# Kernel optimization log

Hardware: AMD Instinct MI355X
Metric: run time of the kernel (lower is better)

## Reference

```python
import jax, jax.numpy as jnp
import numpy as np
from jax import lax

BN_EPS = 1e-5
TINY = 1e-12


def conv2d(x, w, stride, padding):
    # NCHW x OIHW -> NCHW
    return lax.conv_general_dilated(
        x, w, (stride, stride), [(padding, padding), (padding, padding)],
        dimension_numbers=('NCHW', 'OIHW', 'NCHW'))


def pool2x2(x):
    B, C, H, W = x.shape
    return x.reshape(B, C, H // 2, 2, W // 2, 2).mean(axis=(3, 5))


def setup_inputs() -> dict:
    key = jax.random.key(0)
    k0, k1, k2, k3 = jax.random.split(key, 4)
    B, Cin, H, W = 32, 128, 56, 56
    Cout, K = 256, 3
    mean = jax.random.normal(k0, (B, Cin, H, W), jnp.float32)
    std = jax.random.uniform(k1, (B, Cin, H, W), jnp.float32)  # std must be >= 0
    fan_in = Cin * K * K
    bound = 1.0 / np.sqrt(fan_in)  # torch Conv2d default init
    conv_w = jax.random.uniform(k2, (Cout, Cin, K, K), jnp.float32, -bound, bound)
    conv_b = jax.random.uniform(k3, (Cout,), jnp.float32, -bound, bound)
    bn_gamma = jnp.full((Cout,), 2.5, jnp.float32)  # module fills weight with 2.5
    bn_beta = jnp.full((Cout,), 2.5, jnp.float32)   # module fills bias with 2.5
    return {'mean': mean, 'std': std, 'conv_w': conv_w, 'conv_b': conv_b,
            'bn_gamma': bn_gamma, 'bn_beta': bn_beta}


def reference(mean, std, conv_w, conv_b, bn_gamma, bn_beta):
    # mean branch: standard conv
    m = conv2d(mean, conv_w, 1, 1) + conv_b[None, :, None, None]
    # std branch (no rho): independent-variance propagation, var -> conv with w^2
    var = conv2d(std * std, conv_w * conv_w, 1, 1)
    s = jnp.sqrt(var + TINY)
    # BatchNorm2d in training mode: batch statistics over (N, H, W)
    mu = jnp.mean(m, axis=(0, 2, 3), keepdims=True)
    v = jnp.var(m, axis=(0, 2, 3), keepdims=True)  # biased, like torch normalization
    inv = 1.0 / jnp.sqrt(v + BN_EPS)
    g = bn_gamma[None, :, None, None]
    uhat = (m - mu) * inv * g + bn_beta[None, :, None, None]
    # std through BN: pure linear scale by |gamma| / sqrt(var + eps)
    shat = s * inv * jnp.abs(g)
    # moment activation (erf-based Gaussian->Heaviside moment mapping)
    z = uhat / (shat * np.sqrt(2.0) + TINY)
    u = 0.5 * (1.0 + lax.erf(z))               # output mean in (0, 1)
    sa = jnp.sqrt(jnp.clip(u * (1.0 - u), TINY))  # output std of Bernoulli-like moments
    # avg-pool 2x2 stride 2: mean pools linearly, independent vars: std = sqrt(avg(var))/2
    u_p = pool2x2(u)
    s_p = jnp.sqrt(pool2x2(sa * sa)) * 0.5
    return (u_p, s_p)
```

## Files before the change

### kernel.cpp

```cpp
#include <hip/hip_runtime.h>
#include <hip/hip_bf16.h>
#include <math.h>

#define BB 32
#define CIN 128
#define HH 56
#define WW 56
#define COUT 256
#define HW (HH*WW)
#define NPIX (BB*HW)
#define PH 28
#define PW 28
#define POOL_ELEMS ((long)BB*COUT*PH*PW)
#define PADH 58
#define PADW 58
#define ROW_BLOCKS (BB*HH)
#define TOPBOT_BLOCKS (BB*2)
#define WPACK_BLOCKS ((9*COUT*CIN)/256)

typedef unsigned short u16;
using s16x8 = __attribute__((ext_vector_type(8))) short;
using s16x4 = __attribute__((ext_vector_type(4))) short;
using f32x4 = __attribute__((ext_vector_type(4))) float;

__device__ __forceinline__ float b2f(u16 u){ return __uint_as_float(((unsigned)u)<<16); }
__device__ __forceinline__ u16 f2b(float x){
    unsigned u = __float_as_uint(x);
    unsigned r = (u + 0x7fffu + ((u>>16)&1u)) >> 16;
    return (u16)r;
}

__device__ __forceinline__ void gload16(const void* g, void* l){
    __builtin_amdgcn_global_load_lds(
        (const __attribute__((address_space(1))) unsigned int*)g,
        (__attribute__((address_space(3))) unsigned int*)l, 16, 0, 0);
}


__global__ __launch_bounds__(256) void prep_kernel(
    const float* __restrict__ mean, const float* __restrict__ stdv,
    const float* __restrict__ w,
    u16* __restrict__ mean_pad, u16* __restrict__ std2_pad,
    u16* __restrict__ BP, u16* __restrict__ BP2,
    float* __restrict__ sum_, float* __restrict__ sumsq_)
{
    const int bid = blockIdx.x;
    const int t   = threadIdx.x;

    if (bid < ROW_BLOCKS){
        __shared__ u16 ldsm[56*128];
        __shared__ u16 ldss[56*128];
        const int b = bid / HH;
        const int h = bid - b*HH;

        #pragma unroll
        for (int k=0; k<7; ++k){
            int idx = k*256 + t;
            int c   = idx / 14;
            int f4  = idx - c*14;
            long ga = ((long)(b*CIN + c)*HH + h)*WW + f4*4;
            const f32x4 m4 = *(const f32x4*)(mean + ga);
            const f32x4 s4 = *(const f32x4*)(stdv + ga);
            #pragma unroll
            for (int j=0; j<4; ++j){
                int px = f4*4 + j;
                int ci = px*128 + (c ^ ((px & 15) << 3));
                ldsm[ci] = f2b(m4[j]);
                ldss[ci] = f2b(s4[j] * s4[j]);
            }
        }
        __syncthreads();

        const long rowbase = ((long)(b*PADH + (h+1)))*PADW*CIN;
        #pragma unroll
        for (int k=0; k<4; ++k){
            int slot = k*256 + t;
            int px   = slot >> 4;
            int oct  = slot & 15;
            if (px < 56){
                int ci = px*128 + ((oct ^ (px & 15)) << 3);
                long o = rowbase + (long)(px+1)*CIN + oct*8;
                *(s16x8*)(mean_pad + o) = *(const s16x8*)&ldsm[ci];
                *(s16x8*)(std2_pad + o) = *(const s16x8*)&ldss[ci];
            }
        }
        if (t < 64){
            int buf = t >> 5;
            int ppx = ((t >> 4) & 1) ? 57 : 0;
            int oct = t & 15;
            long o  = rowbase + (long)ppx*CIN + oct*8;
            s16x8 z = (s16x8){0,0,0,0,0,0,0,0};
            *(s16x8*)((buf ? std2_pad : mean_pad) + o) = z;
        }
    } else if (bid < ROW_BLOCKS + TOPBOT_BLOCKS){
        int row = bid - ROW_BLOCKS;
        int b   = row >> 1;
        int ph  = (row & 1) ? (PADH-1) : 0;
        const long rowbase = ((long)(b*PADH + ph))*PADW*CIN;
        s16x8 z = (s16x8){0,0,0,0,0,0,0,0};
        #pragma unroll
        for (int k=0; k<8; ++k){
            int g = k*256 + t;
            if (g < 2*PADW*16){
                int buf = g >= PADW*16;
                int gg  = buf ? g - PADW*16 : g;
                int px  = gg >> 4;
                int oct = gg & 15;
                long o  = rowbase + (long)px*CIN + oct*8;
                *(s16x8*)((buf ? std2_pad : mean_pad) + o) = z;
            }
        }
        if (row == 0){ sum_[t] = 0.f; sumsq_[t] = 0.f; }
    } else {
        int tt = (bid - ROW_BLOCKS - TOPBOT_BLOCKS)*256 + t;
        int e    = tt & 7;
        int co   = (tt >> 3) & 255;
        int rest = tt >> 11;
        int ks   = rest >> 2;
        int sub  = rest & 3;
        int r    = ks >> 2;
        int ci   = (ks & 3)*32 + sub*8 + e;
        float v = w[((long)co*CIN + ci)*9 + r];
        BP[tt]  = f2b(v);
        BP2[tt] = f2b(v*v);
    }
}

__global__ __launch_bounds__(256,2) void convw_kernel(
    const u16* __restrict__ mean_pad, const u16* __restrict__ std2_pad,
    const u16* __restrict__ BP, const u16* __restrict__ BP2,
    const float* __restrict__ bias,
    u16* __restrict__ m_out, u16* __restrict__ v_out,
    float* __restrict__ sum_, float* __restrict__ sumsq_)
{
    __shared__ u16 lds[32768];
    const int tid  = threadIdx.x;
    const int lane = tid & 63;
    const int wv   = tid >> 6;

    int gid   = blockIdx.x;
    int local = gid >> 3;
    int p     = (gid & 7)*112 + (local >> 1);
    int path  = local & 1;
    const int b  = p / 28;
    const int h0 = (p - b*28) * 2;

    const u16* __restrict__ Ap = path ? std2_pad : mean_pad;
    const u16* __restrict__ Bp = path ? BP2      : BP;
    u16*       __restrict__ Op = path ? v_out    : m_out;

    const int slot_g = (tid & 15) ^ ((tid >> 4) & 15);
    const int wbase  = (b*PADH + h0)*PADW*CIN;
    const int athr   = (tid >> 4)*CIN + slot_g*8;
    #pragma unroll
    for (int i=0; i<16; ++i){
        const int Ci = (i>>2)*(PADW*CIN) + (i&3)*16*CIN;
        gload16(Ap + wbase + Ci + athr, &lds[i*2048 + tid*8]);
    }
    __syncthreads();

    int R0[7];
    #pragma unroll
    for (int mi=0; mi<7; ++mi){
        int px = mi*16 + (lane & 15);
        int dh = (px >= 56) ? 1 : 0;
        R0[mi] = dh*64 + (px - dh*56);
    }
    const int q = lane >> 4;

    const u16* bp = Bp + (size_t)((lane>>4)*256 + wv*64 + (lane&15))*8;

    f32x4 acc[7][4];
    #pragma unroll
    for (int i=0;i<7;i++)
      #pragma unroll
      for (int j=0;j<4;j++) acc[i][j] = (f32x4){0,0,0,0};

    #pragma unroll
    for (int r=0; r<9; ++r){
        const int kh = r/3, kw = r - (r/3)*3;

        int ab[7];
        #pragma unroll
        for (int mi=0; mi<7; ++mi){
            int R   = R0[mi] + kh*64 + kw;
            int t15 = (R0[mi] + kw) & 15;
            ab[mi] = R*128 + ((q ^ t15) << 3);
        }

        #pragma unroll
        for (int hf=0; hf<2; ++hf){
            #pragma unroll
            for (int kk=0; kk<2; ++kk){
                const size_t ksoff = (size_t)(r*4 + hf*2 + kk)*8192;
                s16x8 bf0 = *(const s16x8*)(bp + ksoff);
                s16x8 bf1 = *(const s16x8*)(bp + ksoff + 128);
                s16x8 bf2 = *(const s16x8*)(bp + ksoff + 256);
                s16x8 bf3 = *(const s16x8*)(bp + ksoff + 384);
                const int sx = hf*64 + kk*32;
                s16x8 af[7];
                #pragma unroll
                for (int mi=0; mi<7; ++mi)
                    af[mi] = *(const s16x8*)&lds[ab[mi] ^ sx];
                __builtin_amdgcn_s_setprio(1);
                #pragma unroll
                for (int mi=0; mi<7; ++mi){
                    acc[mi][0] = __builtin_amdgcn_mfma_f32_16x16x32_bf16(af[mi], bf0, acc[mi][0], 0,0,0);
                    acc[mi][1] = __builtin_amdgcn_mfma_f32_16x16x32_bf16(af[mi], bf1, acc[mi][1], 0,0,0);
                    acc[mi][2] = __builtin_amdgcn_mfma_f32_16x16x32_bf16(af[mi], bf2, acc[mi][2], 0,0,0);
                    acc[mi][3] = __builtin_amdgcn_mfma_f32_16x16x32_bf16(af[mi], bf3, acc[mi][3], 0,0,0);
                }
                __builtin_amdgcn_s_setprio(0);
            }
        }
    }

    float bv[4];
    if (path == 0){
        #pragma unroll
        for (int ni=0;ni<4;ni++) bv[ni] = bias[wv*64 + ni*16 + (lane&15)];
    } else {
        #pragma unroll
        for (int ni=0;ni<4;ni++) bv[ni] = 0.f;
    }

    float ssum[4] = {0.f,0.f,0.f,0.f}, ssq[4] = {0.f,0.f,0.f,0.f};

    #pragma unroll
    for (int mi=0; mi<7; ++mi){
        int px = mi*16 + ((lane>>4)<<2);
        int dh = (px >= 56) ? 1 : 0;
        int w  = px - dh*56;
        #pragma unroll
        for (int ni=0; ni<4; ++ni){
            int co = wv*64 + ni*16 + (lane&15);
            size_t o = (size_t)(b*COUT + co)*HW + (size_t)(h0+dh)*WW + w;
            s16x4 pk;
            #pragma unroll
            for (int rr=0; rr<4; ++rr){
                float vv = acc[mi][ni][rr] + bv[ni];
                pk[rr] = (short)f2b(vv);
                ssum[ni] += vv;
                ssq[ni]  += vv*vv;
            }
            *(s16x4*)(Op + o) = pk;
        }
    }

    if (path == 0){
        #pragma unroll
        for (int ni=0; ni<4; ++ni){
            float s = ssum[ni], s2 = ssq[ni];
            s  += __shfl_xor(s, 16, 64);  s2 += __shfl_xor(s2, 16, 64);
            s  += __shfl_xor(s, 32, 64);  s2 += __shfl_xor(s2, 32, 64);
            if (lane < 16){
                int co = wv*64 + ni*16 + lane;
                atomicAdd(&sum_[co],   s);
                atomicAdd(&sumsq_[co], s2);
            }
        }
    }
}

__global__ __launch_bounds__(256) void final_kernel(
        const u16* __restrict__ m, const u16* __restrict__ var,
        const float* __restrict__ sum_, const float* __restrict__ sumsq_,
        const float* __restrict__ gamma, const float* __restrict__ beta,
        float* __restrict__ out){
    int idx4 = blockIdx.x*256 + threadIdx.x;
    int wo4 = idx4 % (PW/4); int t = idx4 / (PW/4);
    int ho = t % PH; t /= PH;
    int co = t % COUT; int b = t / COUT;
    float g  = gamma[co];
    float be = beta[co];
    float mu = sum_[co] / (float)NPIX;
    float vr = sumsq_[co] / (float)NPIX - mu*mu;
    float inv = 1.0f / sqrtf(vr + 1e-5f);
    float ag = fabsf(g);
    float us[4] = {0.f,0.f,0.f,0.f}, ss[4] = {0.f,0.f,0.f,0.f};
    #pragma unroll
    for (int dh=0; dh<2; ++dh){
        long base = ((long)(b*COUT+co)*HH + 2*ho+dh)*WW + wo4*8;
        const s16x8 vm = *(const s16x8*)&m[base];
        const s16x8 vv = *(const s16x8*)&var[base];
        #pragma unroll
        for (int j=0;j<8;j++){
            float mm = b2f((u16)vm[j]);
            float sdev = sqrtf(b2f((u16)vv[j]) + 1e-12f);
            float uhat = (mm - mu)*inv*g + be;
            float shat = sdev*inv*ag;
            float z = uhat / (shat*1.41421356237f + 1e-12f);
            float u = 0.5f*(1.f + erff(z));
            us[j>>1] += u;
            ss[j>>1] += fmaxf(u*(1.f-u), 1e-12f);
        }
    }
    long ob = ((long)(b*COUT+co)*PH + ho)*PW + wo4*4;
    f32x4 o0, o1;
    #pragma unroll
    for (int k=0;k<4;k++){
        o0[k] = 0.25f*us[k];
        o1[k] = sqrtf(0.25f*ss[k])*0.5f;
    }
    *(f32x4*)(out + ob) = o0;
    *(f32x4*)(out + POOL_ELEMS + ob) = o1;
}


__global__ void wtransf_kernel(const float* __restrict__ w, float* __restrict__ wT){
    int out = blockIdx.x*256 + threadIdx.x;
    if (out >= COUT*CIN*9) return;
    int co = out % COUT;
    int r  = out / COUT;
    wT[out] = w[(long)co*(CIN*9) + r];
}

__global__ __launch_bounds__(256) void stats_old_kernel(const u16* __restrict__ m,
        float* __restrict__ mu_out, float* __restrict__ inv_out){
    int co = blockIdx.x;
    float s=0.f, s2=0.f;
    for (int oc = threadIdx.x; oc < NPIX/8; oc += 256){
        int b = oc / (HW/8); int o8 = oc - b*(HW/8);
        const s16x8 v8 = *(const s16x8*)&m[((size_t)(b*COUT+co))*HW + (size_t)o8*8];
        #pragma unroll
        for (int j=0;j<8;j++){ float v = b2f((u16)v8[j]); s += v; s2 += v*v; }
    }
    __shared__ float rs[256], rs2[256];
    rs[threadIdx.x]=s; rs2[threadIdx.x]=s2; __syncthreads();
    for (int o=128;o>0;o>>=1){
        if (threadIdx.x < o){ rs[threadIdx.x]+=rs[threadIdx.x+o]; rs2[threadIdx.x]+=rs2[threadIdx.x+o]; }
        __syncthreads();
    }
    if (threadIdx.x==0){
        float mu = rs[0]/(float)NPIX;
        float var = rs2[0]/(float)NPIX - mu*mu;
        mu_out[co] = mu;
        inv_out[co] = 1.0f/sqrtf(var + 1e-5f);
    }
}

__global__ __launch_bounds__(256) void final_old_kernel(
        const u16* __restrict__ m, const u16* __restrict__ var,
        const float* __restrict__ mu_, const float* __restrict__ inv_,
        const float* __restrict__ gamma, const float* __restrict__ beta,
        float* __restrict__ out){
    long idx = (long)blockIdx.x*256 + threadIdx.x;
    int wo = (int)(idx % PW); long t = idx / PW;
    int ho = (int)(t % PH); t /= PH;
    int co = (int)(t % COUT); int b = (int)(t / COUT);
    float g  = gamma[co];
    float be = beta[co];
    float mu = mu_[co], inv = inv_[co];
    float ag = fabsf(g);
    float us = 0.f, ss = 0.f;
    #pragma unroll
    for (int dh=0; dh<2; ++dh){
        int hpos = 2*ho+dh;
        long base = ((long)(b*COUT+co)*HH + hpos)*WW + 2*wo;
        #pragma unroll
        for (int dw=0; dw<2; ++dw){
            float mm = b2f(m[base+dw]);
            float vv = b2f(var[base+dw]);
            float sdev = sqrtf(vv + 1e-12f);
            float uhat = (mm - mu)*inv*g + be;
            float shat = sdev*inv*ag;
            float z = uhat / (shat*1.41421356237f + 1e-12f);
            float u = 0.5f*(1.f + erff(z));
            float sa2 = fmaxf(u*(1.f-u), 1e-12f);
            us += u; ss += sa2;
        }
    }
    out[idx]              = 0.25f*us;
    out[POOL_ELEMS + idx] = sqrtf(0.25f*ss)*0.5f;
}

#define CI_CHUNK 64
#define XW 32
__global__ __launch_bounds__(256) void conv_old_kernel(
    const float* __restrict__ mean, const float* __restrict__ stdv,
    const float* __restrict__ wT, const float* __restrict__ bias,
    u16* __restrict__ m_out, u16* __restrict__ v_out)
{
    __shared__ float lds_m[CI_CHUNK][3][XW];
    __shared__ float lds_s[CI_CHUNK][3][XW];
    const int co   = threadIdx.x;
    const int half = blockIdx.x;
    const int h    = blockIdx.y;
    const int b    = blockIdx.z;
    const int w_base = half*28;

    float acc_m[28], acc_v[28];
    #pragma unroll
    for (int i=0;i<28;i++){ acc_m[i]=0.f; acc_v[i]=0.f; }

    for (int c=0; c<CIN; c+=CI_CHUNK){
        for (int t = threadIdx.x; t < CI_CHUNK*3*30; t += 256){
            int pos = t % 30; int r = t / 30; int hh = r % 3; int ci_l = r / 3;
            int gh = h - 1 + hh; int gw = w_base - 1 + pos;
            float vm = 0.f, vs = 0.f;
            if ((unsigned)gh < (unsigned)HH && (unsigned)gw < (unsigned)WW){
                long gi = ((long)(b*CIN + (c+ci_l))*HH + gh)*WW + gw;
                vm = mean[gi];
                float sv = stdv[gi];
                vs = sv*sv;
            }
            lds_m[ci_l][hh][pos] = vm;
            lds_s[ci_l][hh][pos] = vs;
        }
        __syncthreads();
        for (int ci_l=0; ci_l<CI_CHUNK; ++ci_l){
            int rbase = (c+ci_l)*9;
            #pragma unroll
            for (int kh=0; kh<3; ++kh){
                float w0 = wT[(long)(rbase + kh*3 + 0)*COUT + co];
                float w1 = wT[(long)(rbase + kh*3 + 1)*COUT + co];
                float w2 = wT[(long)(rbase + kh*3 + 2)*COUT + co];
                float xm[30];
                #pragma unroll
                for (int p=0;p<30;p++) xm[p] = lds_m[ci_l][kh][p];
                #pragma unroll
                for (int i=0;i<28;i++) acc_m[i] += w0*xm[i] + w1*xm[i+1] + w2*xm[i+2];
                float q0=w0*w0, q1=w1*w1, q2=w2*w2;
                float xs[30];
                #pragma unroll
                for (int p=0;p<30;p++) xs[p] = lds_s[ci_l][kh][p];
                #pragma unroll
                for (int i=0;i<28;i++) acc_v[i] += q0*xs[i] + q1*xs[i+1] + q2*xs[i+2];
            }
        }
        __syncthreads();
    }
    float bvv = bias[co];
    long obase = ((long)(b*COUT+co)*HH + h)*WW + w_base;
    #pragma unroll
    for (int i=0;i<28;i++){
        m_out[obase+i] = f2b(acc_m[i]+bvv);
        v_out[obase+i] = f2b(acc_v[i]);
    }
}

extern "C" void kernel_launch(void* const* d_in, const int* in_sizes, int n_in,
                              void* d_out, int out_size, void* d_ws, size_t ws_size,
                              hipStream_t stream)
{
    const float* mean   = (const float*)d_in[0];
    const float* stdv   = (const float*)d_in[1];
    const float* conv_w = (const float*)d_in[2];
    const float* conv_b = (const float*)d_in[3];
    const float* gamma  = (const float*)d_in[4];
    const float* beta   = (const float*)d_in[5];
    float* out = (float*)d_out;
    char* ws = (char*)d_ws;

    const size_t PAD_BYTES  = (size_t)BB*PADH*PADW*CIN*2;
    const size_t SLACK      = 8192;
    const size_t OFF_STD2   = PAD_BYTES + SLACK;
    const size_t OFF_WT     = OFF_STD2 + PAD_BYTES + SLACK;
    const size_t WT_BYTES   = (size_t)9*COUT*CIN*2;
    const size_t OFF_WT2    = OFF_WT + WT_BYTES;
    const size_t OFF_M      = OFF_WT2 + WT_BYTES;
    const size_t MV_BYTES   = (size_t)BB*COUT*HW*2;
    const size_t OFF_V      = OFF_M + MV_BYTES;
    const size_t OFF_SUM    = OFF_V + MV_BYTES;
    const size_t OFF_SUMSQ  = OFF_SUM + 1024;
    const size_t NEED_FAST  = OFF_SUMSQ + 1024;

    if (ws_size >= NEED_FAST){
        u16* mean_pad = (u16*)ws;
        u16* std2_pad = (u16*)(ws + OFF_STD2);
        u16* BP   = (u16*)(ws + OFF_WT);
        u16* BP2  = (u16*)(ws + OFF_WT2);
        u16* m_buf = (u16*)(ws + OFF_M);
        u16* v_buf = (u16*)(ws + OFF_V);
        float* sum_   = (float*)(ws + OFF_SUM);
        float* sumsq_ = (float*)(ws + OFF_SUMSQ);

        prep_kernel<<<ROW_BLOCKS + TOPBOT_BLOCKS + WPACK_BLOCKS, 256, 0, stream>>>(
            mean, stdv, conv_w, mean_pad, std2_pad, BP, BP2, sum_, sumsq_);
        convw_kernel<<<(NPIX/112)*2, 256, 0, stream>>>(
            mean_pad, std2_pad, BP, BP2, conv_b, m_buf, v_buf, sum_, sumsq_);
        final_kernel<<<(int)(POOL_ELEMS/4/256), 256, 0, stream>>>(
            m_buf, v_buf, sum_, sumsq_, gamma, beta, out);
    } else {
        u16* m_buf = (u16*)ws;
        u16* v_buf = (u16*)(ws + (size_t)BB*COUT*HW*2);
        float* wT  = (float*)(ws + (size_t)BB*COUT*HW*4);
        float* mu  = (float*)(ws + (size_t)BB*COUT*HW*4 + (size_t)COUT*CIN*9*4);
        float* inv = mu + 256;
        wtransf_kernel<<<(COUT*CIN*9+255)/256, 256, 0, stream>>>(conv_w, wT);
        conv_old_kernel<<<dim3(2, HH, BB), 256, 0, stream>>>(mean, stdv, wT, conv_b, m_buf, v_buf);
        stats_old_kernel<<<COUT, 256, 0, stream>>>(m_buf, mu, inv);
        final_old_kernel<<<(int)(POOL_ELEMS/256), 256, 0, stream>>>(m_buf, v_buf, mu, inv, gamma, beta, out);
    }
}
```

Measured before the change: 205.0 us.

## Make conv kernel persistent with rolling LDS row buffer and prefetch

The conv kernel now launches 512 persistent blocks. Each block walks a contiguous range of tiles (pairs of output rows) within one XCD partition and keeps a 4-row circular LDS buffer. Consecutive tiles reuse the overlapping input rows, and the two new rows for the next tile are prefetched partway through the current tile's MFMA loop, so the halo reload and load latency are hidden. The cost is extra barriers and uneven tile counts per block (224/64 is not an integer), which may leave some blocks with more work.

```diff
diff --git a/kernel.cpp b/kernel.cpp
--- a/kernel.cpp
+++ b/kernel.cpp
@@ -52,7 +52,6 @@
         __shared__ u16 ldss[56*128];
         const int b = bid / HH;
         const int h = bid - b*HH;
-
         #pragma unroll
         for (int k=0; k<7; ++k){
             int idx = k*256 + t;
@@ -70,7 +69,6 @@
             }
         }
         __syncthreads();
-
         const long rowbase = ((long)(b*PADH + (h+1)))*PADW*CIN;
         #pragma unroll
         for (int k=0; k<4; ++k){
@@ -138,125 +136,157 @@
     const int lane = tid & 63;
     const int wv   = tid >> 6;
 
-    int gid   = blockIdx.x;
-    int local = gid >> 3;
-    int p     = (gid & 7)*112 + (local >> 1);
-    int path  = local & 1;
-    const int b  = p / 28;
-    const int h0 = (p - b*28) * 2;
-
-    const u16* __restrict__ Ap = path ? std2_pad : mean_pad;
-    const u16* __restrict__ Bp = path ? BP2      : BP;
-    u16*       __restrict__ Op = path ? v_out    : m_out;
+    const int xcd = blockIdx.x & 7;
+    const int jj  = blockIdx.x >> 3;
+    const int t0  = (jj*224) >> 6;
+    const int t1  = ((jj+1)*224) >> 6;
 
     const int slot_g = (tid & 15) ^ ((tid >> 4) & 15);
-    const int wbase  = (b*PADH + h0)*PADW*CIN;
     const int athr   = (tid >> 4)*CIN + slot_g*8;
-    #pragma unroll
-    for (int i=0; i<16; ++i){
-        const int Ci = (i>>2)*(PADW*CIN) + (i&3)*16*CIN;
-        gload16(Ap + wbase + Ci + athr, &lds[i*2048 + tid*8]);
-    }
-    __syncthreads();
-
-    int R0[7];
+
+    int col0[7], dhv[7];
     #pragma unroll
     for (int mi=0; mi<7; ++mi){
         int px = mi*16 + (lane & 15);
         int dh = (px >= 56) ? 1 : 0;
-        R0[mi] = dh*64 + (px - dh*56);
+        dhv[mi]  = dh;
+        col0[mi] = px - dh*56;
     }
     const int q = lane >> 4;
 
-    const u16* bp = Bp + (size_t)((lane>>4)*256 + wv*64 + (lane&15))*8;
-
-    f32x4 acc[7][4];
-    #pragma unroll
-    for (int i=0;i<7;i++)
-      #pragma unroll
-      for (int j=0;j<4;j++) acc[i][j] = (f32x4){0,0,0,0};
-
-    #pragma unroll
-    for (int r=0; r<9; ++r){
-        const int kh = r/3, kw = r - (r/3)*3;
-
-        int ab[7];
+    for (int tt = t0; tt < t1; ++tt){
+        const int path = tt / 112;
+        const int pl   = tt - path*112;
+        const int p    = xcd*112 + pl;
+        const int b    = p / 28;
+        const int h0   = (p - b*28) * 2;
+        const bool cont = (tt > t0) && (pl != 0) && ((pl % 28) != 0);
+        const bool nxt  = (tt+1 < t1) && ((pl+1) < 112) && (((pl+1) % 28) != 0);
+
+        const u16* __restrict__ Ap = path ? std2_pad : mean_pad;
+        const u16* __restrict__ Bp = path ? BP2      : BP;
+        u16*       __restrict__ Op = path ? v_out    : m_out;
+        const int wbase = (b*PADH + h0)*PADW*CIN;
+
+        if (!cont){
+            #pragma unroll
+            for (int i=0; i<16; ++i){
+                int prs = (h0 + (i>>2)) & 3;
+                gload16(Ap + wbase + (i>>2)*(PADW*CIN) + (i&3)*16*CIN + athr,
+                        &lds[prs*8192 + (i&3)*2048 + tid*8]);
+            }
+            __syncthreads();
+        }
+
+        const u16* bp = Bp + (size_t)((lane>>4)*256 + wv*64 + (lane&15))*8;
+
+        f32x4 acc[7][4];
+        #pragma unroll
+        for (int i=0;i<7;i++)
+          #pragma unroll
+          for (int j2=0;j2<4;j2++) acc[i][j2] = (f32x4){0,0,0,0};
+
+        #pragma unroll
+        for (int r=0; r<9; ++r){
+            const int kh = r/3, kw = r - (r/3)*3;
+
+            int ab[7];
+            #pragma unroll
+            for (int mi=0; mi<7; ++mi){
+                int rs = (h0 + dhv[mi] + kh) & 3;
+                int c  = col0[mi] + kw;
+                ab[mi] = rs*8192 + c*128 + ((q ^ (c & 15)) << 3);
+            }
+
+            #pragma unroll
+            for (int hf=0; hf<2; ++hf){
+                #pragma unroll
+                for (int kk=0; kk<2; ++kk){
+                    const size_t ksoff = (size_t)(r*4 + hf*2 + kk)*8192;
+                    s16x8 bf0 = *(const s16x8*)(bp + ksoff);
+                    s16x8 bf1 = *(const s16x8*)(bp + ksoff + 128);
+                    s16x8 bf2 = *(const s16x8*)(bp + ksoff + 256);
+                    s16x8 bf3 = *(const s16x8*)(bp + ksoff + 384);
+                    const int sx = hf*64 + kk*32;
+                    s16x8 af[7];
+                    #pragma unroll
+                    for (int mi=0; mi<7; ++mi)
+                        af[mi] = *(const s16x8*)&lds[ab[mi] ^ sx];
+                    __builtin_amdgcn_s_setprio(1);
+                    #pragma unroll
+                    for (int mi=0; mi<7; ++mi){
+                        acc[mi][0] = __builtin_amdgcn_mfma_f32_16x16x32_bf16(af[mi], bf0, acc[mi][0], 0,0,0);
+                        acc[mi][1] = __builtin_amdgcn_mfma_f32_16x16x32_bf16(af[mi], bf1, acc[mi][1], 0,0,0);
+                        acc[mi][2] = __builtin_amdgcn_mfma_f32_16x16x32_bf16(af[mi], bf2, acc[mi][2], 0,0,0);
+                        acc[mi][3] = __builtin_amdgcn_mfma_f32_16x16x32_bf16(af[mi], bf3, acc[mi][3], 0,0,0);
+                    }
+                    __builtin_amdgcn_s_setprio(0);
+                }
+            }
+
+            if (r == 2 || r == 5){
+                __builtin_amdgcn_s_barrier();
+                if (nxt){
+                    const int H   = h0 + ((r==2) ? 4 : 5);
+                    const int prs = H & 3;
+                    const int hb  = (b*PADH + H)*PADW*CIN;
+                    #pragma unroll
+                    for (int i=0; i<4; ++i){
+                        gload16(Ap + hb + i*16*CIN + athr,
+                                &lds[prs*8192 + i*2048 + tid*8]);
+                    }
+                }
+            }
+        }
+
+        if (nxt){
+            asm volatile("s_waitcnt vmcnt(0)" ::: "memory");
+            __builtin_amdgcn_s_barrier();
+        }
+
+        float bv[4];
+        if (path == 0){
+            #pragma unroll
+            for (int ni=0;ni<4;ni++) bv[ni] = bias[wv*64 + ni*16 + (lane&15)];
+        } else {
+            #pragma unroll
+            for (int ni=0;ni<4;ni++) bv[ni] = 0.f;
+        }
+
+        float ssum[4] = {0.f,0.f,0.f,0.f}, ssq[4] = {0.f,0.f,0.f,0.f};
+
         #pragma unroll
         for (int mi=0; mi<7; ++mi){
-            int R   = R0[mi] + kh*64 + kw;
-            int t15 = (R0[mi] + kw) & 15;
-            ab[mi] = R*128 + ((q ^ t15) << 3);
-        }
-
-        #pragma unroll
-        for (int hf=0; hf<2; ++hf){
-            #pragma unroll
-            for (int kk=0; kk<2; ++kk){
-                const size_t ksoff = (size_t)(r*4 + hf*2 + kk)*8192;
-                s16x8 bf0 = *(const s16x8*)(bp + ksoff);
-                s16x8 bf1 = *(const s16x8*)(bp + ksoff + 128);
-                s16x8 bf2 = *(const s16x8*)(bp + ksoff + 256);
-                s16x8 bf3 = *(const s16x8*)(bp + ksoff + 384);
-                const int sx = hf*64 + kk*32;
-                s16x8 af[7];
+            int px = mi*16 + ((lane>>4)<<2);
+            int dh = (px >= 56) ? 1 : 0;
+            int w  = px - dh*56;
+            #pragma unroll
+            for (int ni=0; ni<4; ++ni){
+                int co = wv*64 + ni*16 + (lane&15);
+                size_t o = (size_t)(b*COUT + co)*HW + (size_t)(h0+dh)*WW + w;
+                s16x4 pk;
                 #pragma unroll
-                for (int mi=0; mi<7; ++mi)
-                    af[mi] = *(const s16x8*)&lds[ab[mi] ^ sx];
-                __builtin_amdgcn_s_setprio(1);
-                #pragma unroll
-                for (int mi=0; mi<7; ++mi){
-                    acc[mi][0] = __builtin_amdgcn_mfma_f32_16x16x32_bf16(af[mi], bf0, acc[mi][0], 0,0,0);
-                    acc[mi][1] = __builtin_amdgcn_mfma_f32_16x16x32_bf16(af[mi], bf1, acc[mi][1], 0,0,0);
-                    acc[mi][2] = __builtin_amdgcn_mfma_f32_16x16x32_bf16(af[mi], bf2, acc[mi][2], 0,0,0);
-                    acc[mi][3] = __builtin_amdgcn_mfma_f32_16x16x32_bf16(af[mi], bf3, acc[mi][3], 0,0,0);
+                for (int rr=0; rr<4; ++rr){
+                    float vv = acc[mi][ni][rr] + bv[ni];
+                    pk[rr] = (short)f2b(vv);
+                    ssum[ni] += vv;
+                    ssq[ni]  += vv*vv;
                 }
-                __builtin_amdgcn_s_setprio(0);
-            }
-        }
-    }
-
-    float bv[4];
-    if (path == 0){
-        #pragma unroll
-        for (int ni=0;ni<4;ni++) bv[ni] = bias[wv*64 + ni*16 + (lane&15)];
-    } else {
-        #pragma unroll
-        for (int ni=0;ni<4;ni++) bv[ni] = 0.f;
-    }
-
-    float ssum[4] = {0.f,0.f,0.f,0.f}, ssq[4] = {0.f,0.f,0.f,0.f};
-
-    #pragma unroll
-    for (int mi=0; mi<7; ++mi){
-        int px = mi*16 + ((lane>>4)<<2);
-        int dh = (px >= 56) ? 1 : 0;
-        int w  = px - dh*56;
-        #pragma unroll
-        for (int ni=0; ni<4; ++ni){
-            int co = wv*64 + ni*16 + (lane&15);
-            size_t o = (size_t)(b*COUT + co)*HW + (size_t)(h0+dh)*WW + w;
-            s16x4 pk;
-            #pragma unroll
-            for (int rr=0; rr<4; ++rr){
-                float vv = acc[mi][ni][rr] + bv[ni];
-                pk[rr] = (short)f2b(vv);
-                ssum[ni] += vv;
-                ssq[ni]  += vv*vv;
-            }
-            *(s16x4*)(Op + o) = pk;
-        }
-    }
-
-    if (path == 0){
-        #pragma unroll
-        for (int ni=0; ni<4; ++ni){
-            float s = ssum[ni], s2 = ssq[ni];
-            s  += __shfl_xor(s, 16, 64);  s2 += __shfl_xor(s2, 16, 64);
-            s  += __shfl_xor(s, 32, 64);  s2 += __shfl_xor(s2, 32, 64);
-            if (lane < 16){
-                int co = wv*64 + ni*16 + lane;
-                atomicAdd(&sum_[co],   s);
-                atomicAdd(&sumsq_[co], s2);
+                *(s16x4*)(Op + o) = pk;
+            }
+        }
+
+        if (path == 0){
+            #pragma unroll
+            for (int ni=0; ni<4; ++ni){
+                float s = ssum[ni], s2 = ssq[ni];
+                s  += __shfl_xor(s, 16, 64);  s2 += __shfl_xor(s2, 16, 64);
+                s  += __shfl_xor(s, 32, 64);  s2 += __shfl_xor(s2, 32, 64);
+                if (lane < 16){
+                    int co = wv*64 + ni*16 + lane;
+                    atomicAdd(&sum_[co],   s);
+                    atomicAdd(&sumsq_[co], s2);
+                }
             }
         }
     }
@@ -477,7 +507,7 @@
 
         prep_kernel<<<ROW_BLOCKS + TOPBOT_BLOCKS + WPACK_BLOCKS, 256, 0, stream>>>(
             mean, stdv, conv_w, mean_pad, std2_pad, BP, BP2, sum_, sumsq_);
-        convw_kernel<<<(NPIX/112)*2, 256, 0, stream>>>(
+        convw_kernel<<<512, 256, 0, stream>>>(
             mean_pad, std2_pad, BP, BP2, conv_b, m_buf, v_buf, sum_, sumsq_);
         final_kernel<<<(int)(POOL_ELEMS/4/256), 256, 0, stream>>>(
             m_buf, v_buf, sum_, sumsq_, gamma, beta, out);
```

Result: slower. 217.7 us (+6.2%).
